# Performance work log

Measured on AMD Instinct MI355X. Metric: run time of the kernel, lower is better.

The kernel has to match this reference:

```python
import jax, jax.numpy as jnp
import numpy as np

P = 7      # local_patch_size
H = 6      # heads
DH = 30    # dim_head


def setup_inputs() -> dict:
    key = jax.random.key(0)
    ks = jax.random.split(key, 5)
    b, dim, L = 16, 180, 14336
    inner = H * DH  # 180
    fmap = jax.random.normal(ks[0], (b, dim, L), dtype=jnp.float32)
    Wq = jax.random.normal(ks[1], (inner, dim), dtype=jnp.float32) * 0.05
    Wkv = jax.random.normal(ks[2], (2 * inner, dim), dtype=jnp.float32) * 0.05
    Wo = jax.random.normal(ks[3], (dim, inner), dtype=jnp.float32) * 0.05
    bo = jax.random.normal(ks[4], (dim,), dtype=jnp.float32) * 0.05
    return {"fmap": fmap, "Wq": Wq, "Wkv": Wkv, "Wo": Wo, "bo": bo}


def reference(fmap, Wq, Wkv, Wo, bo):
    b, c, L = fmap.shape
    l = L // P
    scale = DH ** -0.5
    # 'b c (l p) -> b c l p' windows
    x = fmap.reshape(b, c, l, P)
    # pointwise (kernel-1) conv projections
    q = jnp.einsum('ec,bclp->belp', Wq, x)
    kv = jnp.einsum('ec,bclp->belp', Wkv, x)
    k, v = jnp.split(kv, 2, axis=1)

    def split_heads(t):
        # (b, h*d, l, p) -> (b, l, h, p, d)
        return t.reshape(b, H, DH, l, P).transpose(0, 3, 1, 4, 2)

    q, k, v = map(split_heads, (q, k, v))
    dots = jnp.einsum('blhid,blhjd->blhij', q, k) * scale  # per-window 7x7 scores
    attn = jax.nn.softmax(dots, axis=-1)
    out = jnp.einsum('blhij,blhjd->blhid', attn, v)  # (b, l, h, p, d)
    # '(b l h) p d -> b (h d) (l p)'
    out = out.transpose(0, 2, 4, 1, 3).reshape(b, H * DH, l * P)
    return jnp.einsum('oe,bel->bol', Wo, out) + bo[None, :, None]
```

## Files before the change

kernel.cpp:

```cpp
#include <hip/hip_runtime.h>
#include <stdint.h>

namespace {

constexpr int DIM  = 180;
constexpr int LL   = 14336;
constexpr int B    = 16;
constexpr int T    = 112;
constexpr int NCH  = 128;
constexpr int EQKV = 540;
constexpr int EPAD = 192;

constexpr int QT_STRIDE = 584;
constexpr int XS_STRIDE = 200;

typedef __attribute__((ext_vector_type(8))) short bf16x8;
typedef __attribute__((ext_vector_type(4))) float f32x4;

union Frag { bf16x8 v; uint32_t u[4]; unsigned short s[8]; };

__device__ __forceinline__ unsigned short f2b(float f) {
  uint32_t u = __builtin_bit_cast(uint32_t, f);
  u = (u + 0x7fffu + ((u >> 16) & 1u)) >> 16;
  return (unsigned short)u;
}
__device__ __forceinline__ float blo(uint32_t u) { return __builtin_bit_cast(float, u << 16); }
__device__ __forceinline__ float bhi(uint32_t u) { return __builtin_bit_cast(float, u & 0xffff0000u); }
__device__ __forceinline__ f32x4 zero4() { f32x4 z = {0.f,0.f,0.f,0.f}; return z; }

__device__ __forceinline__ bf16x8 zfrag() {
  Frag f; f.u[0]=f.u[1]=f.u[2]=f.u[3]=0u; return f.v;
}

}

__global__ __launch_bounds__(1024) void la_prep(
    const float* __restrict__ Wq, const float* __restrict__ Wkv,
    const float* __restrict__ Wo, unsigned short* __restrict__ wqkv_b,
    unsigned short* __restrict__ wo_b) {
  const int idx = (int)(blockIdx.x * 1024 + threadIdx.x);
  if (idx < EQKV * EPAD) {
    const int e = idx / EPAD, c = idx - e * EPAD;
    float v = 0.f;
    if (c < DIM) v = (e < DIM) ? Wq[e * DIM + c] : Wkv[(size_t)(e - DIM) * DIM + c];
    wqkv_b[idx] = f2b(v);
  } else {
    const int k = idx - EQKV * EPAD;
    if (k < DIM * EPAD) {
      const int o = k / EPAD, cc = k - o * EPAD;
      const int h = cc >> 5, d = cc & 31;
      float v = 0.f;
      if (d < 30) v = Wo[o * DIM + h * 30 + d];
      wo_b[k] = f2b(v);
    }
  }
}

__global__ __launch_bounds__(1024) void la_main(
    const float* __restrict__ fmap, const unsigned short* __restrict__ wqkv,
    const unsigned short* __restrict__ wo_b, const float* __restrict__ bo,
    float* __restrict__ out) {
  __shared__ unsigned short qt[T * QT_STRIDE];
  __shared__ unsigned short xs[64 * XS_STRIDE];

  const int tid  = (int)threadIdx.x;
  const int wave = tid >> 6;
  const int lane = tid & 63;
  const int l15  = lane & 15;
  const int g    = lane >> 4;

  const int bi    = (int)blockIdx.x;
  const int b     = bi >> 7;
  const int chunk = bi & 127;
  const int t0    = chunk * T;

#pragma unroll
  for (int ph = 0; ph < 2; ++ph) {
    const int tb = ph ? 64 : 0;
    const int tn = ph ? 48 : 64;
    const int n0 = ph ? 4 : 0;
    const int NT = ph ? 3 : 4;
    __syncthreads();
    const int nt4 = tn >> 2;
    for (int idx = tid; idx < 192 * nt4; idx += 1024) {
      const int c  = idx / nt4;
      const int t4 = idx - c * nt4;
      const int t  = t4 * 4;
      float4 v = {0.f, 0.f, 0.f, 0.f};
      if (c < DIM)
        v = *(const float4*)(fmap + (size_t)(b * DIM + c) * LL + (t0 + tb + t));
      xs[(t + 0) * XS_STRIDE + c] = f2b(v.x);
      xs[(t + 1) * XS_STRIDE + c] = f2b(v.y);
      xs[(t + 2) * XS_STRIDE + c] = f2b(v.z);
      xs[(t + 3) * XS_STRIDE + c] = f2b(v.w);
    }
    __syncthreads();
    for (int mt = wave; mt < 36; mt += 16) {
      f32x4 acc[4];
#pragma unroll
      for (int n = 0; n < 4; ++n) acc[n] = zero4();
      const int e_a = mt * 16 + l15;
#pragma unroll
      for (int ks = 0; ks < 6; ++ks) {
        const int c0 = ks * 32 + g * 8;
        const bf16x8 a = (e_a < EQKV) ? *(const bf16x8*)(wqkv + (size_t)e_a * EPAD + c0)
                                      : zfrag();
#pragma unroll
        for (int n = 0; n < 4; ++n) {
          if (n < NT) {
            const int trow = (n0 + n) * 16 + l15 - tb;
            const bf16x8 bf = *(const bf16x8*)(xs + trow * XS_STRIDE + c0);
            acc[n] = __builtin_amdgcn_mfma_f32_16x16x32_bf16(a, bf, acc[n], 0, 0, 0);
          }
        }
      }
#pragma unroll
      for (int n = 0; n < 4; ++n) {
        if (n < NT) {
          const int t = (n0 + n) * 16 + l15;
#pragma unroll
          for (int r = 0; r < 4; ++r) {
            const int e = mt * 16 + g * 4 + r;
            if (e < EQKV) {
              const int part = (e >= 360) ? 2 : ((e >= DIM) ? 1 : 0);
              const int rr = e - part * DIM;
              const int h = rr / 30;
              const int d = rr - h * 30;
              qt[t * QT_STRIDE + part * EPAD + h * 32 + d] = f2b(acc[n][r]);
            }
          }
        }
      }
    }
  }
  __syncthreads();

  if (tid < 672) {
    const float scale = 0.18257418583505536f;
    const int w   = tid / 42;
    const int rem = tid - w * 42;
    const int h   = rem / 7;
    const int i   = rem - h * 7;
    const int ti  = w * 7 + i;
    const uint32_t* qrow = (const uint32_t*)(qt + ti * QT_STRIDE + h * 32);
    const unsigned short* kbase = qt + (w * 7) * QT_STRIDE + EPAD + h * 32;
    float dots[7];
#pragma unroll
    for (int j = 0; j < 7; ++j) dots[j] = 0.f;
#pragma unroll
    for (int dp = 0; dp < 15; ++dp) {
      const uint32_t qu = qrow[dp];
      const float q0 = blo(qu), q1 = bhi(qu);
#pragma unroll
      for (int j = 0; j < 7; ++j) {
        const uint32_t ku = *(const uint32_t*)(kbase + j * QT_STRIDE + dp * 2);
        dots[j] += q0 * blo(ku);
        dots[j] += q1 * bhi(ku);
      }
    }
    float mx = dots[0];
#pragma unroll
    for (int j = 1; j < 7; ++j) mx = fmaxf(mx, dots[j]);
    float aw[7];
    float s = 0.f;
#pragma unroll
    for (int j = 0; j < 7; ++j) {
      const float pj = __expf(scale * (dots[j] - mx));
      aw[j] = pj; s += pj;
    }
    const float inv = 1.f / s;
#pragma unroll
    for (int j = 0; j < 7; ++j) aw[j] *= inv;
    const unsigned short* vbase = qt + (w * 7) * QT_STRIDE + 2 * EPAD + h * 32;
    uint32_t* orow = (uint32_t*)(qt + ti * QT_STRIDE + h * 32);
#pragma unroll
    for (int dp = 0; dp < 15; ++dp) {
      float o0 = 0.f, o1 = 0.f;
#pragma unroll
      for (int j = 0; j < 7; ++j) {
        const uint32_t vu = *(const uint32_t*)(vbase + j * QT_STRIDE + dp * 2);
        o0 += aw[j] * blo(vu);
        o1 += aw[j] * bhi(vu);
      }
      orow[dp] = (uint32_t)f2b(o0) | ((uint32_t)f2b(o1) << 16);
    }
    orow[15] = 0u;
  }
  __syncthreads();

  for (int p = wave; p < 84; p += 16) {
    const int m = p / 7;
    const int n = p - m * 7;
    f32x4 acc = zero4();
    const int o_a = m * 16 + l15;
    const int t_b = n * 16 + l15;
#pragma unroll
    for (int ks = 0; ks < 6; ++ks) {
      const int c0 = ks * 32 + g * 8;
      const bf16x8 a = (o_a < DIM) ? *(const bf16x8*)(wo_b + (size_t)o_a * EPAD + c0)
                                   : zfrag();
      const bf16x8 bf = *(const bf16x8*)(qt + t_b * QT_STRIDE + c0);
      acc = __builtin_amdgcn_mfma_f32_16x16x32_bf16(a, bf, acc, 0, 0, 0);
    }
#pragma unroll
    for (int r = 0; r < 4; ++r) {
      const int o = m * 16 + g * 4 + r;
      if (o < DIM) {
        const int t = n * 16 + l15;
        out[(size_t)(b * DIM + o) * LL + t0 + t] = acc[r] + bo[o];
      }
    }
  }
}

extern "C" void kernel_launch(void* const* d_in, const int* in_sizes, int n_in,
                              void* d_out, int out_size, void* d_ws, size_t ws_size,
                              hipStream_t stream) {
  const float* fmap = (const float*)d_in[0];
  const float* Wq   = (const float*)d_in[1];
  const float* Wkv  = (const float*)d_in[2];
  const float* Wo   = (const float*)d_in[3];
  const float* bo   = (const float*)d_in[4];
  float* o = (float*)d_out;

  unsigned short* wqkv_b = (unsigned short*)d_ws;
  unsigned short* wo_b   = wqkv_b + EQKV * EPAD;

  const int prep_elems = EQKV * EPAD + DIM * EPAD;
  hipLaunchKernelGGL(la_prep, dim3((prep_elems + 1023) / 1024), dim3(1024), 0,
                     stream, Wq, Wkv, Wo, wqkv_b, wo_b);
  hipLaunchKernelGGL(la_main, dim3(B * NCH), dim3(1024), 0, stream,
                     fmap, wqkv_b, wo_b, bo, o);
}
```

Baseline: 408.1 us.

## Halve tile to 56 tokens per block with 512 threads for higher occupancy

Cuts each block's token tile from 112 to 56 (8 windows) and the block size from 1024 to 512 threads, doubling the grid and shrinking LDS per block so more blocks can be resident per CU. The QKV projection is restructured into two 32-token phases with two MFMA accumulators per wave, and the per-element head/part index math is replaced by an LDS lookup table built at block start. The trade-off is that Wqkv and Wo fragments are reloaded from global/L2 twice as often per token, and the padded last 16-token column in the output GEMM does wasted work.

New measurement: 401.3 us. About the same (-1.7%).

```diff
diff --git a/kernel.cpp b/kernel.cpp
--- a/kernel.cpp
+++ b/kernel.cpp
@@ -6,13 +6,16 @@
 constexpr int DIM  = 180;
 constexpr int LL   = 14336;
 constexpr int B    = 16;
-constexpr int T    = 112;
-constexpr int NCH  = 128;
+constexpr int T    = 56;
+constexpr int NCH  = 256;
 constexpr int EQKV = 540;
 constexpr int EPAD = 192;
 
 constexpr int QT_STRIDE = 584;
 constexpr int XS_STRIDE = 200;
+constexpr int QT_U16  = T * QT_STRIDE;
+constexpr int XS_U16  = 32 * XS_STRIDE;
+constexpr int LDS_U16 = QT_U16 + XS_U16 + 544;
 
 typedef __attribute__((ext_vector_type(8))) short bf16x8;
 typedef __attribute__((ext_vector_type(4))) float f32x4;
@@ -24,10 +27,12 @@
   u = (u + 0x7fffu + ((u >> 16) & 1u)) >> 16;
   return (unsigned short)u;
 }
+__device__ __forceinline__ uint32_t pack2(float lo, float hi) {
+  return (uint32_t)f2b(lo) | ((uint32_t)f2b(hi) << 16);
+}
 __device__ __forceinline__ float blo(uint32_t u) { return __builtin_bit_cast(float, u << 16); }
 __device__ __forceinline__ float bhi(uint32_t u) { return __builtin_bit_cast(float, u & 0xffff0000u); }
 __device__ __forceinline__ f32x4 zero4() { f32x4 z = {0.f,0.f,0.f,0.f}; return z; }
-
 __device__ __forceinline__ bf16x8 zfrag() {
   Frag f; f.u[0]=f.u[1]=f.u[2]=f.u[3]=0u; return f.v;
 }
@@ -56,12 +61,14 @@
   }
 }
 
-__global__ __launch_bounds__(1024) void la_main(
+__global__ __launch_bounds__(512, 4) void la_main(
     const float* __restrict__ fmap, const unsigned short* __restrict__ wqkv,
     const unsigned short* __restrict__ wo_b, const float* __restrict__ bo,
     float* __restrict__ out) {
-  __shared__ unsigned short qt[T * QT_STRIDE];
-  __shared__ unsigned short xs[64 * XS_STRIDE];
+  __shared__ unsigned short lds[LDS_U16];
+  unsigned short* qt  = lds;
+  unsigned short* xs  = lds + QT_U16;
+  unsigned short* lut = xs + XS_U16;
 
   const int tid  = (int)threadIdx.x;
   const int wave = tid >> 6;
@@ -70,72 +77,68 @@
   const int g    = lane >> 4;
 
   const int bi    = (int)blockIdx.x;
-  const int b     = bi >> 7;
-  const int chunk = bi & 127;
+  const int b     = bi >> 8;
+  const int chunk = bi & 255;
   const int t0    = chunk * T;
 
+  for (int e = tid; e < EQKV; e += 512) {
+    const int part = (e >= 360) ? 2 : ((e >= DIM) ? 1 : 0);
+    const int rr = e - part * DIM;
+    const int h = rr / 30;
+    const int d = rr - h * 30;
+    lut[e] = (unsigned short)(part * EPAD + h * 32 + d);
+  }
+
 #pragma unroll
   for (int ph = 0; ph < 2; ++ph) {
-    const int tb = ph ? 64 : 0;
-    const int tn = ph ? 48 : 64;
-    const int n0 = ph ? 4 : 0;
-    const int NT = ph ? 3 : 4;
+    const int tb = ph * 32;
     __syncthreads();
-    const int nt4 = tn >> 2;
-    for (int idx = tid; idx < 192 * nt4; idx += 1024) {
-      const int c  = idx / nt4;
-      const int t4 = idx - c * nt4;
-      const int t  = t4 * 4;
+#pragma unroll
+    for (int it = 0; it < 3; ++it) {
+      const int idx = tid + it * 512;
+      const int c  = idx >> 3;
+      const int tl = (idx & 7) * 4;
       float4 v = {0.f, 0.f, 0.f, 0.f};
-      if (c < DIM)
-        v = *(const float4*)(fmap + (size_t)(b * DIM + c) * LL + (t0 + tb + t));
-      xs[(t + 0) * XS_STRIDE + c] = f2b(v.x);
-      xs[(t + 1) * XS_STRIDE + c] = f2b(v.y);
-      xs[(t + 2) * XS_STRIDE + c] = f2b(v.z);
-      xs[(t + 3) * XS_STRIDE + c] = f2b(v.w);
+      if (c < DIM && (tb + tl) < T)
+        v = *(const float4*)(fmap + (size_t)(b * DIM + c) * LL + t0 + tb + tl);
+      unsigned short* xr = xs + tl * XS_STRIDE + c;
+      xr[0 * XS_STRIDE] = f2b(v.x);
+      xr[1 * XS_STRIDE] = f2b(v.y);
+      xr[2 * XS_STRIDE] = f2b(v.z);
+      xr[3 * XS_STRIDE] = f2b(v.w);
     }
     __syncthreads();
-    for (int mt = wave; mt < 36; mt += 16) {
-      f32x4 acc[4];
-#pragma unroll
-      for (int n = 0; n < 4; ++n) acc[n] = zero4();
+    for (int mt = wave; mt < 36; mt += 8) {
       const int e_a = mt * 16 + l15;
+      f32x4 acc0 = zero4(), acc1 = zero4();
 #pragma unroll
       for (int ks = 0; ks < 6; ++ks) {
         const int c0 = ks * 32 + g * 8;
-        const bf16x8 a = (e_a < EQKV) ? *(const bf16x8*)(wqkv + (size_t)e_a * EPAD + c0)
-                                      : zfrag();
-#pragma unroll
-        for (int n = 0; n < 4; ++n) {
-          if (n < NT) {
-            const int trow = (n0 + n) * 16 + l15 - tb;
-            const bf16x8 bf = *(const bf16x8*)(xs + trow * XS_STRIDE + c0);
-            acc[n] = __builtin_amdgcn_mfma_f32_16x16x32_bf16(a, bf, acc[n], 0, 0, 0);
-          }
+        const bf16x8 a = (e_a < EQKV)
+            ? *(const bf16x8*)(wqkv + (size_t)e_a * EPAD + c0) : zfrag();
+        const bf16x8 b0 = *(const bf16x8*)(xs + l15 * XS_STRIDE + c0);
+        const bf16x8 b1 = *(const bf16x8*)(xs + (16 + l15) * XS_STRIDE + c0);
+        acc0 = __builtin_amdgcn_mfma_f32_16x16x32_bf16(a, b0, acc0, 0, 0, 0);
+        acc1 = __builtin_amdgcn_mfma_f32_16x16x32_bf16(a, b1, acc1, 0, 0, 0);
+      }
+      const int e0 = mt * 16 + g * 4;
+#pragma unroll
+      for (int nt = 0; nt < 2; ++nt) {
+        const f32x4 A = nt ? acc1 : acc0;
+        const int t = tb + nt * 16 + l15;
+        if (t < T) {
+          unsigned short* qrow = qt + t * QT_STRIDE;
+          if (e0 + 0 < EQKV) qrow[lut[e0 + 0]] = f2b(A[0]);
+          if (e0 + 1 < EQKV) qrow[lut[e0 + 1]] = f2b(A[1]);
+          if (e0 + 2 < EQKV) qrow[lut[e0 + 2]] = f2b(A[2]);
+          if (e0 + 3 < EQKV) qrow[lut[e0 + 3]] = f2b(A[3]);
         }
       }
-#pragma unroll
-      for (int n = 0; n < 4; ++n) {
-        if (n < NT) {
-          const int t = (n0 + n) * 16 + l15;
-#pragma unroll
-          for (int r = 0; r < 4; ++r) {
-            const int e = mt * 16 + g * 4 + r;
-            if (e < EQKV) {
-              const int part = (e >= 360) ? 2 : ((e >= DIM) ? 1 : 0);
-              const int rr = e - part * DIM;
-              const int h = rr / 30;
-              const int d = rr - h * 30;
-              qt[t * QT_STRIDE + part * EPAD + h * 32 + d] = f2b(acc[n][r]);
-            }
-          }
-        }
-      }
     }
   }
   __syncthreads();
 
-  if (tid < 672) {
+  if (tid < 336) {
     const float scale = 0.18257418583505536f;
     const int w   = tid / 42;
     const int rem = tid - w * 42;
@@ -182,32 +185,33 @@
         o0 += aw[j] * blo(vu);
         o1 += aw[j] * bhi(vu);
       }
-      orow[dp] = (uint32_t)f2b(o0) | ((uint32_t)f2b(o1) << 16);
+      orow[dp] = pack2(o0, o1);
     }
     orow[15] = 0u;
   }
   __syncthreads();
 
-  for (int p = wave; p < 84; p += 16) {
-    const int m = p / 7;
-    const int n = p - m * 7;
+  for (int p = wave; p < 48; p += 8) {
+    const int m = p >> 2;
+    const int n = p & 3;
+    const int o_a  = m * 16 + l15;
+    const int tcol = n * 16 + l15;
+    const int trd  = (tcol < T) ? tcol : (T - 1);
     f32x4 acc = zero4();
-    const int o_a = m * 16 + l15;
-    const int t_b = n * 16 + l15;
 #pragma unroll
     for (int ks = 0; ks < 6; ++ks) {
       const int c0 = ks * 32 + g * 8;
-      const bf16x8 a = (o_a < DIM) ? *(const bf16x8*)(wo_b + (size_t)o_a * EPAD + c0)
-                                   : zfrag();
-      const bf16x8 bf = *(const bf16x8*)(qt + t_b * QT_STRIDE + c0);
+      const bf16x8 a = (o_a < DIM)
+          ? *(const bf16x8*)(wo_b + (size_t)o_a * EPAD + c0) : zfrag();
+      const bf16x8 bf = *(const bf16x8*)(qt + trd * QT_STRIDE + c0);
       acc = __builtin_amdgcn_mfma_f32_16x16x32_bf16(a, bf, acc, 0, 0, 0);
     }
-#pragma unroll
-    for (int r = 0; r < 4; ++r) {
-      const int o = m * 16 + g * 4 + r;
-      if (o < DIM) {
-        const int t = n * 16 + l15;
-        out[(size_t)(b * DIM + o) * LL + t0 + t] = acc[r] + bo[o];
+    if (tcol < T) {
+#pragma unroll
+      for (int r = 0; r < 4; ++r) {
+        const int o = m * 16 + g * 4 + r;
+        if (o < DIM)
+          out[(size_t)(b * DIM + o) * LL + t0 + tcol] = acc[r] + bo[o];
       }
     }
   }
@@ -229,6 +233,6 @@
   const int prep_elems = EQKV * EPAD + DIM * EPAD;
   hipLaunchKernelGGL(la_prep, dim3((prep_elems + 1023) / 1024), dim3(1024), 0,
                      stream, Wq, Wkv, Wo, wqkv_b, wo_b);
-  hipLaunchKernelGGL(la_main, dim3(B * NCH), dim3(1024), 0, stream,
+  hipLaunchKernelGGL(la_main, dim3(B * NCH), dim3(512), 0, stream,
                      fmap, wqkv_b, wo_b, bo, o);
 }
```
